# Kernel tuning notes

Measured on AMD Instinct MI355X. Metric: run time of the kernel, lower is better.

## Reference

```python
import jax, jax.numpy as jnp
import numpy as np

B, C, N, H = 8, 256, 1024, 8

def setup_inputs() -> dict:
    key = jax.random.key(0)
    ks = jax.random.split(key, 6)
    x = jax.random.normal(ks[0], (B, C, 3, N), jnp.float32)
    scale = 1.0 / np.sqrt(C).astype(np.float32)
    Wq = jax.random.normal(ks[1], (C, C), jnp.float32) * scale
    Wk = jax.random.normal(ks[2], (C, C), jnp.float32) * scale
    Wv = jax.random.normal(ks[3], (C, C), jnp.float32) * scale
    Wp = jax.random.normal(ks[4], (C, C), jnp.float32) * scale
    mask = jax.random.randint(ks[5], (B, N), 0, 2).astype(bool)  # True = padded
    return {"x": x, "Wq": Wq, "Wk": Wk, "Wv": Wv, "Wp": Wp, "mask": mask}

def _vn_linear(W, x):
    # VNLinear: channel-mixing linear (no bias) over the C axis of [B, C, 3, N]
    return jnp.einsum('oc,bcdn->bodn', W, x)

def _to_heads(t):
    # [B, C, 3, N] -> [B, H, N, (C//H)*3]
    hd = C // H
    return t.reshape(B, H, hd, 3, N).transpose(0, 1, 4, 2, 3).reshape(B, H, N, hd * 3)

def reference(x, Wq, Wk, Wv, Wp, mask):
    hd = C // H
    D = hd * 3
    q = _to_heads(_vn_linear(Wq, x))
    k = _to_heads(_vn_linear(Wk, x))
    v = _to_heads(_vn_linear(Wv, x))
    att = jnp.einsum('bhnd,bhmd->bhnm', q, k) * (1.0 / np.sqrt(D).astype(np.float32))
    att = jnp.where(mask[:, None, None, :], -jnp.inf, att)
    att = jax.nn.softmax(att, axis=-1)
    y = jnp.einsum('bhnm,bhmd->bhnd', att, v)
    # [B, H, N, D] -> [B, H, D, N] -> [B, H, hd, 3, N] -> [B, C, 3, N]
    y = y.transpose(0, 1, 3, 2).reshape(B, H, hd, 3, N).reshape(B, C, 3, N)
    return _vn_linear(Wp, y)
```

## Files before the change

kernel.cpp:

```cpp
#include <hip/hip_runtime.h>
#include <hip/hip_bf16.h>
#include <math.h>

#define B_ 8
#define C_ 256
#define N_ 1024
#define H_ 8
#define DH 96
#define BHN (C_*3*N_)
#define SC 0.10206207261596575f
#define SCL2 0.14722193f

typedef _Float16 half8 __attribute__((ext_vector_type(8)));
typedef float f32x4 __attribute__((ext_vector_type(4)));
typedef float f32x16 __attribute__((ext_vector_type(16)));

typedef __attribute__((address_space(1))) void gvoid;
typedef __attribute__((address_space(3))) void lvoid;
__device__ inline void gl_lds16(const _Float16* g, _Float16* l) {
  __builtin_amdgcn_global_load_lds((gvoid*)g, (lvoid*)l, 16, 0, 0);
}

__device__ inline float ex2(float x) { return __builtin_amdgcn_exp2f(x); }

typedef __fp16 fp16x2 __attribute__((ext_vector_type(2)));
union H2U { fp16x2 h2; unsigned u; };
__device__ inline unsigned pkh(float a, float b) {
  H2U x; x.h2 = __builtin_amdgcn_cvt_pkrtz(a, b); return x.u;
}
union PF { half8 v; unsigned u[4]; };

__device__ inline void plswap(unsigned& a, unsigned& b) {
  asm volatile("v_permlane32_swap_b32 %0, %1" : "+v"(a), "+v"(b));
}

__global__ __launch_bounds__(256) void prep_kernel(
    const float* __restrict__ x, _Float16* __restrict__ XT,
    const float* __restrict__ Wq, const float* __restrict__ Wk,
    const float* __restrict__ Wv, const float* __restrict__ Wp,
    _Float16* __restrict__ Wh, const unsigned* __restrict__ mraw,
    unsigned long long* __restrict__ mb) {
  if (blockIdx.z == 8) {
    int bid = blockIdx.y * 48 + blockIdx.x;
    if (bid < 128) {
      int idx = bid * 256 + threadIdx.x;
      int e0 = idx * 8;
      const float* src = (e0 < 65536) ? Wq
                       : (e0 < 131072) ? Wk
                       : (e0 < 196608) ? Wv : Wp;
      int off = e0 & 65535;
      float4 a = *(const float4*)&src[off];
      float4 b = *(const float4*)&src[off + 4];
      _Float16 t[8] = {(_Float16)a.x, (_Float16)a.y, (_Float16)a.z,
                       (_Float16)a.w, (_Float16)b.x, (_Float16)b.y,
                       (_Float16)b.z, (_Float16)b.w};
      *(uint4*)&Wh[e0] = *(uint4*)t;
    } else if (bid == 128) {
      __shared__ int notI, notF;
      if (threadIdx.x == 0) { notI = 0; notF = 0; }
      __syncthreads();
      int li = 0, lf = 0;
      for (int i = threadIdx.x; i < 2048; i += 256) {
        unsigned w = mraw[i];
        if (w > 1u) li = 1;
        if (w != 0u && w != 0x3F800000u) lf = 1;
      }
      if (li) atomicOr(&notI, 1);
      if (lf) atomicOr(&notF, 1);
      __syncthreads();
      const int tid = threadIdx.x;
      if (tid < 128) {
        int base = tid * 64;
        unsigned long long bits = 0;
        if (!notI) {
          for (int j = 0; j < 64; ++j)
            bits |= (unsigned long long)(mraw[base + j] & 1u) << j;
        } else if (!notF) {
          for (int j = 0; j < 64; ++j)
            bits |= (unsigned long long)(mraw[base + j] != 0u ? 1 : 0) << j;
        } else {
          const unsigned char* m8 = (const unsigned char*)mraw;
          for (int j = 0; j < 64; ++j)
            bits |= (unsigned long long)(m8[base + j] ? 1 : 0) << j;
        }
        mb[tid] = bits;
      }
    }
    return;
  }

  __shared__ _Float16 T[64][65];
  const int m0 = blockIdx.x * 64;
  const int c0 = blockIdx.y * 64;
  const int b = blockIdx.z;
  const float* xb = x + (size_t)b * BHN;
  _Float16* ob = XT + (size_t)b * BHN;
  const int t = threadIdx.x;
#pragma unroll
  for (int i = 0; i < 16; ++i) {
    int e = t + i * 256;
    int c = e >> 6, m = e & 63;
    T[m][c] = (_Float16)xb[(size_t)(c0 + c) * 3072 + m0 + m];
  }
  __syncthreads();
#pragma unroll
  for (int i = 0; i < 2; ++i) {
    int e = t + i * 256;
    int m = e >> 3, ch = e & 7;
    _Float16 tmp[8];
#pragma unroll
    for (int j = 0; j < 8; ++j) tmp[j] = T[m][ch * 8 + j];
    *(uint4*)&ob[(size_t)(m0 + m) * 256 + c0 + ch * 8] = *(uint4*)tmp;
  }
}

template <int MODE>
__global__ __launch_bounds__(256, 4) void mgemm_kernel(
    const _Float16* __restrict__ Wh, int woff,
    const _Float16* __restrict__ Xn,
    _Float16* __restrict__ O0, _Float16* __restrict__ O1,
    _Float16* __restrict__ O2, float* __restrict__ Of, int nw) {
  const int zz = blockIdx.z;
  const int w = zz % nw;
  const int b = zz / nw;
  const _Float16* Wb = Wh + (size_t)(woff + w) * 65536;
  const _Float16* Bb = Xn + (size_t)b * BHN;
  const int o0 = blockIdx.y * 128;
  const int bn0 = blockIdx.x * 128;

  __shared__ __align__(16) _Float16 Ah[8192];
  __shared__ __align__(16) _Float16 Bh[8192];

  const int tid = threadIdx.x;
  const int wave = tid >> 6;
  const int lane = tid & 63;
  const int lg = lane >> 4, ll = lane & 15;
  const int wm = wave >> 1, wn = wave & 1;

  f32x4 acc[4][4];
#pragma unroll
  for (int mi = 0; mi < 4; ++mi)
#pragma unroll
    for (int ni = 0; ni < 4; ++ni) acc[mi][ni] = (f32x4){0.f, 0.f, 0.f, 0.f};

  for (int k0 = 0; k0 < 256; k0 += 64) {
#pragma unroll
    for (int i = 0; i < 4; ++i) {
      int e = tid + i * 256;
      int r = e >> 3, cch = e & 7;
      int srcc = cch ^ (r & 7);
      _Float16* dst = &Ah[(size_t)(i * 256 + wave * 64) * 8];
      gl_lds16(Wb + (size_t)(o0 + r) * 256 + k0 + srcc * 8, dst);
      _Float16* dstb = &Bh[(size_t)(i * 256 + wave * 64) * 8];
      gl_lds16(Bb + (size_t)(bn0 + r) * 256 + k0 + srcc * 8, dstb);
    }
    __syncthreads();
#pragma unroll
    for (int kk = 0; kk < 2; ++kk) {
      half8 af[4], bf[4];
#pragma unroll
      for (int mi = 0; mi < 4; ++mi) {
        int row = wm * 64 + mi * 16 + ll;
        int ch = (kk * 4 + lg) ^ (row & 7);
        af[mi] = *(const half8*)&Ah[row * 64 + ch * 8];
      }
#pragma unroll
      for (int ni = 0; ni < 4; ++ni) {
        int row = wn * 64 + ni * 16 + ll;
        int ch = (kk * 4 + lg) ^ (row & 7);
        bf[ni] = *(const half8*)&Bh[row * 64 + ch * 8];
      }
#pragma unroll
      for (int mi = 0; mi < 4; ++mi)
#pragma unroll
        for (int ni = 0; ni < 4; ++ni)
          acc[mi][ni] = __builtin_amdgcn_mfma_f32_16x16x32_f16(
              af[mi], bf[ni], acc[mi][ni], 0, 0, 0);
    }
    __syncthreads();
  }

#pragma unroll
  for (int mi = 0; mi < 4; ++mi) {
#pragma unroll
    for (int ni = 0; ni < 4; ++ni) {
      int o = o0 + wm * 64 + mi * 16 + lg * 4;
      int mcol = bn0 + wn * 64 + ni * 16 + ll;
      if constexpr (MODE == 1) {
        float* Ofb = Of + (size_t)b * BHN;
#pragma unroll
        for (int r = 0; r < 4; ++r)
          Ofb[(size_t)(o + r) * 3072 + mcol] = acc[mi][ni][r];
      } else {
        const int h = o >> 5, i = o & 31;
        const int dd = mcol >> 10, tok = mcol & 1023;
        const size_t bh8 = (size_t)(b * 8 + h);
        if (w == 2) {
          int tt = tok >> 6, kk = tok & 63;
          int kt = kk >> 4, hi2 = (kk >> 3) & 1, e = kk & 7;
          size_t base = ((((bh8 * 16 + tt) * 4 + kt) * 3 + dd) * 512) +
                        (size_t)i * 16 + hi2 * 8 + e;
#pragma unroll
          for (int r = 0; r < 4; ++r)
            O2[base + r * 16] = (_Float16)acc[mi][ni][r];
        } else {
          int dperm = dd * 32 + i;
          int pp = dperm >> 3, j0 = i & 7;
          int ks = pp >> 1, hif = pp & 1;
          float qs = (w == 0) ? SCL2 : 1.0f;
          _Float16 t4[4];
#pragma unroll
          for (int r = 0; r < 4; ++r) t4[r] = (_Float16)(acc[mi][ni][r] * qs);
          size_t idx;
          if (w == 0) {
            idx = ((bh8 * 32 + (tok >> 5)) * 6 + ks) * 512 +
                  (size_t)(tok & 31) * 16 + hif * 8 + j0;
            *(uint2*)&O0[idx] = *(uint2*)t4;
          } else {
            idx = ((bh8 * 16 + (tok >> 6)) * 6 + ks) * 1024 +
                  (size_t)(tok & 63) * 16 + hif * 8 + j0;
            *(uint2*)&O1[idx] = *(uint2*)t4;
          }
        }
      }
    }
  }
}

__global__ __launch_bounds__(256, 2) void attn_kernel(
    const _Float16* __restrict__ Qp, const _Float16* __restrict__ Kp,
    const _Float16* __restrict__ Vp,
    const unsigned long long* __restrict__ mbits,
    _Float16* __restrict__ yT) {
  const int gid = blockIdx.x;
  const int bh = gid & 63;
  const int qt = gid >> 6;
  const int b = bh >> 3, h = bh & 7;
  const int n0 = qt * 128;

  const int tid = threadIdx.x;
  const int lane = tid & 63;
  const int wave = tid >> 6;
  const int hi = lane >> 5;
  const int lq = lane & 31;
  const int wq0 = wave * 32;

  const size_t bh8 = (size_t)(b * 8 + h);
  const int lo16 = lq * 16 + hi * 8;

  const _Float16* Qb = Qp + (bh8 * 32 + (qt * 4 + wave)) * 6 * 512 + lo16;
  half8 qf[6];
#pragma unroll
  for (int ks = 0; ks < 6; ++ks) qf[ks] = *(const half8*)(Qb + ks * 512);

  const _Float16* Kh = Kp + bh8 * 98304 + lo16;
  const _Float16* Vh = Vp + bh8 * 98304 + lo16;

  half8 kf[6][2];
  auto loadK = [&](int t) {
    const _Float16* Kt = Kh + t * 6144;
#pragma unroll
    for (int ks = 0; ks < 6; ++ks) {
      kf[ks][0] = *(const half8*)(Kt + ks * 1024);
      kf[ks][1] = *(const half8*)(Kt + ks * 1024 + 512);
    }
  };
  loadK(0);

  float M = 0.f, Lh = 0.f;
  f32x16 yacc[3];
#pragma unroll
  for (int dt = 0; dt < 3; ++dt)
#pragma unroll
    for (int r = 0; r < 16; ++r) yacc[dt][r] = 0.f;

  for (int t = 0; t < 16; ++t) {
    const _Float16* Vt = Vh + t * 6144;
    half8 vf[4][3];
#pragma unroll
    for (int kt = 0; kt < 4; ++kt)
#pragma unroll
      for (int dt = 0; dt < 3; ++dt)
        vf[kt][dt] = *(const half8*)(Vt + (kt * 3 + dt) * 512);

    const unsigned long long m64 = mbits[b * 16 + t];

    f32x16 s[2];
#pragma unroll
    for (int r = 0; r < 16; ++r) { s[0][r] = 0.f; s[1][r] = 0.f; }
    __builtin_amdgcn_s_setprio(1);
#pragma unroll
    for (int ks = 0; ks < 6; ++ks) {
      s[0] = __builtin_amdgcn_mfma_f32_32x32x16_f16(kf[ks][0], qf[ks], s[0],
                                                    0, 0, 0);
      s[1] = __builtin_amdgcn_mfma_f32_32x32x16_f16(kf[ks][1], qf[ks], s[1],
                                                    0, 0, 0);
    }
    __builtin_amdgcn_s_setprio(0);

    if (t + 1 < 16) loadK(t + 1);

    float mx = -1e30f;
#pragma unroll
    for (int nt = 0; nt < 2; ++nt) {
      unsigned wm = (unsigned)(m64 >> (nt * 32 + 4 * hi));
#pragma unroll
      for (int r = 0; r < 16; ++r) {
        float sv = s[nt][r];
        sv = ((wm >> ((r & 3) + 8 * (r >> 2))) & 1u) ? -1e30f : sv;
        s[nt][r] = sv;
        mx = fmaxf(mx, sv);
      }
    }
    if (__any(mx > M + 12.f)) {
      float mx2 = fmaxf(mx, __shfl_xor(mx, 32));
      float newM = fmaxf(M, mx2);
      float corr = ex2(M - newM);
      M = newM;
      Lh *= corr;
#pragma unroll
      for (int dt = 0; dt < 3; ++dt)
#pragma unroll
        for (int r = 0; r < 16; ++r) yacc[dt][r] *= corr;
    }
    float psum = 0.f;
#pragma unroll
    for (int nt = 0; nt < 2; ++nt)
#pragma unroll
      for (int r = 0; r < 16; ++r) {
        float p = ex2(s[nt][r] - M);
        s[nt][r] = p;
        psum += p;
      }
    Lh += psum;

#pragma unroll
    for (int nt = 0; nt < 2; ++nt) {
#pragma unroll
      for (int hf = 0; hf < 2; ++hf) {
        const int bs = hf * 8;
        unsigned A0 = pkh(s[nt][bs + 0], s[nt][bs + 1]);
        unsigned A1 = pkh(s[nt][bs + 2], s[nt][bs + 3]);
        unsigned B0 = pkh(s[nt][bs + 4], s[nt][bs + 5]);
        unsigned B1 = pkh(s[nt][bs + 6], s[nt][bs + 7]);
        plswap(A0, B0);
        plswap(A1, B1);
        PF pf;
        pf.u[0] = A0;
        pf.u[1] = A1;
        pf.u[2] = B0;
        pf.u[3] = B1;
        const int kt = nt * 2 + hf;
        __builtin_amdgcn_s_setprio(1);
#pragma unroll
        for (int dt = 0; dt < 3; ++dt)
          yacc[dt] = __builtin_amdgcn_mfma_f32_32x32x16_f16(
              vf[kt][dt], pf.v, yacc[dt], 0, 0, 0);
        __builtin_amdgcn_s_setprio(0);
      }
    }
  }

  float L = Lh + __shfl_xor(Lh, 32);
  float inv = (L > 0.f) ? 1.f / L : 0.f;
  _Float16* yb = yT + (size_t)b * BHN;
#pragma unroll
  for (int dt = 0; dt < 3; ++dt) {
    _Float16* rowp =
        yb + (size_t)(dt * 1024 + n0 + wq0 + lq) * 256 + h * 32 + hi * 4;
#pragma unroll
    for (int g = 0; g < 4; ++g) {
      _Float16 t4[4];
#pragma unroll
      for (int j = 0; j < 4; ++j)
        t4[j] = (_Float16)(yacc[dt][g * 4 + j] * inv);
      *(uint2*)(rowp + g * 8) = *(uint2*)t4;
    }
  }
}

extern "C" void kernel_launch(void* const* d_in, const int* in_sizes, int n_in,
                              void* d_out, int out_size, void* d_ws,
                              size_t ws_size, hipStream_t stream) {
  const float* x = (const float*)d_in[0];
  const float* Wq = (const float*)d_in[1];
  const float* Wk = (const float*)d_in[2];
  const float* Wv = (const float*)d_in[3];
  const float* Wp = (const float*)d_in[4];
  const unsigned* mask = (const unsigned*)d_in[5];
  float* out = (float*)d_out;

  _Float16* Wh = (_Float16*)d_ws;
  _Float16* XT = Wh + 4 * 65536;
  _Float16* Qp = XT + (size_t)B_ * BHN;
  _Float16* Kp = Qp + (size_t)B_ * BHN;
  _Float16* Vp = Kp + (size_t)B_ * BHN;
  _Float16* yT = Vp + (size_t)B_ * BHN;
  unsigned long long* mb = (unsigned long long*)(yT + (size_t)B_ * BHN);

  prep_kernel<<<dim3(48, 4, 9), 256, 0, stream>>>(x, XT, Wq, Wk, Wv, Wp, Wh,
                                                  mask, mb);

  dim3 g1(24, 2, B_ * 3);
  mgemm_kernel<0><<<g1, 256, 0, stream>>>(Wh, 0, XT, Qp, Kp, Vp, nullptr, 3);

  attn_kernel<<<dim3(512), 256, 0, stream>>>(Qp, Kp, Vp, mb, yT);

  dim3 g3(24, 2, B_);
  mgemm_kernel<1><<<g3, 256, 0, stream>>>(Wh, 3, yT, nullptr, nullptr, nullptr,
                                          out, 1);
}
```

Measured before the change: 90.29 us.

## Compact unpadded keys/values to front and skip fully masked key tiles

The prep kernel computes a per-batch prefix-sum permutation that places unpadded tokens first and padded tokens last. It also writes the number of non-empty 64-key tiles and per-tile mask bits for that order. The projection GEMM scatters K and V rows into this compacted order, and the attention loop runs only over the live tiles instead of all 16. With about half the keys masked, this roughly halves attention work. It adds a serial scan in one block and indirect index loads in the GEMM epilogue.

Measured after the change: 94.59 us. 1.05x slower.

```diff
diff --git a/kernel.cpp b/kernel.cpp
--- a/kernel.cpp
+++ b/kernel.cpp
@@ -39,11 +39,13 @@
     const float* __restrict__ Wq, const float* __restrict__ Wk,
     const float* __restrict__ Wv, const float* __restrict__ Wp,
     _Float16* __restrict__ Wh, const unsigned* __restrict__ mraw,
-    unsigned long long* __restrict__ mb) {
+    unsigned long long* __restrict__ mb, int* __restrict__ pos,
+    int* __restrict__ ntArr) {
   if (blockIdx.z == 8) {
     int bid = blockIdx.y * 48 + blockIdx.x;
+    const int tid = threadIdx.x;
     if (bid < 128) {
-      int idx = bid * 256 + threadIdx.x;
+      int idx = bid * 256 + tid;
       int e0 = idx * 8;
       const float* src = (e0 < 65536) ? Wq
                        : (e0 < 131072) ? Wk
@@ -57,10 +59,11 @@
       *(uint4*)&Wh[e0] = *(uint4*)t;
     } else if (bid == 128) {
       __shared__ int notI, notF;
-      if (threadIdx.x == 0) { notI = 0; notF = 0; }
+      __shared__ int cnts[256];
+      if (tid == 0) { notI = 0; notF = 0; }
       __syncthreads();
       int li = 0, lf = 0;
-      for (int i = threadIdx.x; i < 2048; i += 256) {
+      for (int i = tid; i < 2048; i += 256) {
         unsigned w = mraw[i];
         if (w > 1u) li = 1;
         if (w != 0u && w != 0x3F800000u) lf = 1;
@@ -68,22 +71,45 @@
       if (li) atomicOr(&notI, 1);
       if (lf) atomicOr(&notF, 1);
       __syncthreads();
-      const int tid = threadIdx.x;
-      if (tid < 128) {
-        int base = tid * 64;
-        unsigned long long bits = 0;
-        if (!notI) {
-          for (int j = 0; j < 64; ++j)
-            bits |= (unsigned long long)(mraw[base + j] & 1u) << j;
-        } else if (!notF) {
-          for (int j = 0; j < 64; ++j)
-            bits |= (unsigned long long)(mraw[base + j] != 0u ? 1 : 0) << j;
-        } else {
-          const unsigned char* m8 = (const unsigned char*)mraw;
-          for (int j = 0; j < 64; ++j)
-            bits |= (unsigned long long)(m8[base + j] ? 1 : 0) << j;
+      const int nI = notI, nF = notF;
+      auto ispad = [&](int idx) -> int {
+        if (!nI) return (int)(mraw[idx] & 1u);
+        if (!nF) return (mraw[idx] != 0u) ? 1 : 0;
+        return ((const unsigned char*)mraw)[idx] ? 1 : 0;
+      };
+      const int gb = tid >> 5, gi = tid & 31;
+      const int tbase = gb * 1024 + gi * 32;
+      int cloc = 0;
+      for (int j = 0; j < 32; ++j) cloc += 1 - ispad(tbase + j);
+      cnts[tid] = cloc;
+      __syncthreads();
+      int pre = 0, tot = 0;
+      for (int k2 = 0; k2 < 32; ++k2) {
+        int v = cnts[gb * 32 + k2];
+        if (k2 < gi) pre += v;
+        tot += v;
+      }
+      int pu = pre;
+      int pm = tot + (gi * 32 - pre);
+      for (int j = 0; j < 32; ++j) {
+        int tok = gi * 32 + j;
+        int pd = ispad(tbase + j);
+        int p = pd ? pm++ : pu++;
+        pos[gb * 1024 + tok] = p;
+      }
+      if (gi == 0) {
+        int nt = (tot + 63) >> 6;
+        if (nt == 0) nt = 1;
+        ntArr[gb] = nt;
+        int rem = tot & 63;
+        for (int t = 0; t < 16; ++t) {
+          unsigned long long bits;
+          if (t < nt - 1) bits = 0ULL;
+          else if (t == nt - 1)
+            bits = (rem == 0 && tot > 0) ? 0ULL : (~0ULL << rem);
+          else bits = ~0ULL;
+          mb[gb * 16 + t] = bits;
         }
-        mb[tid] = bits;
       }
     }
     return;
@@ -117,7 +143,7 @@
 template <int MODE>
 __global__ __launch_bounds__(256, 4) void mgemm_kernel(
     const _Float16* __restrict__ Wh, int woff,
-    const _Float16* __restrict__ Xn,
+    const _Float16* __restrict__ Xn, const int* __restrict__ pos,
     _Float16* __restrict__ O0, _Float16* __restrict__ O1,
     _Float16* __restrict__ O2, float* __restrict__ Of, int nw) {
   const int zz = blockIdx.z;
@@ -196,31 +222,36 @@
         const int dd = mcol >> 10, tok = mcol & 1023;
         const size_t bh8 = (size_t)(b * 8 + h);
         if (w == 2) {
-          int tt = tok >> 6, kk = tok & 63;
+          int ctok = pos[b * 1024 + tok];
+          int tt = ctok >> 6, kk = ctok & 63;
           int kt = kk >> 4, hi2 = (kk >> 3) & 1, e = kk & 7;
           size_t base = ((((bh8 * 16 + tt) * 4 + kt) * 3 + dd) * 512) +
                         (size_t)i * 16 + hi2 * 8 + e;
 #pragma unroll
           for (int r = 0; r < 4; ++r)
             O2[base + r * 16] = (_Float16)acc[mi][ni][r];
+        } else if (w == 1) {
+          int ctok = pos[b * 1024 + tok];
+          int dperm = dd * 32 + i;
+          int pp = dperm >> 3, j0 = i & 7;
+          int ks = pp >> 1, hif = pp & 1;
+          _Float16 t4[4];
+#pragma unroll
+          for (int r = 0; r < 4; ++r) t4[r] = (_Float16)acc[mi][ni][r];
+          size_t idx = ((bh8 * 16 + (ctok >> 6)) * 6 + ks) * 1024 +
+                       (size_t)(ctok & 63) * 16 + hif * 8 + j0;
+          *(uint2*)&O1[idx] = *(uint2*)t4;
         } else {
           int dperm = dd * 32 + i;
           int pp = dperm >> 3, j0 = i & 7;
           int ks = pp >> 1, hif = pp & 1;
-          float qs = (w == 0) ? SCL2 : 1.0f;
           _Float16 t4[4];
 #pragma unroll
-          for (int r = 0; r < 4; ++r) t4[r] = (_Float16)(acc[mi][ni][r] * qs);
-          size_t idx;
-          if (w == 0) {
-            idx = ((bh8 * 32 + (tok >> 5)) * 6 + ks) * 512 +
-                  (size_t)(tok & 31) * 16 + hif * 8 + j0;
-            *(uint2*)&O0[idx] = *(uint2*)t4;
-          } else {
-            idx = ((bh8 * 16 + (tok >> 6)) * 6 + ks) * 1024 +
-                  (size_t)(tok & 63) * 16 + hif * 8 + j0;
-            *(uint2*)&O1[idx] = *(uint2*)t4;
-          }
+          for (int r = 0; r < 4; ++r)
+            t4[r] = (_Float16)(acc[mi][ni][r] * SCL2);
+          size_t idx = ((bh8 * 32 + (tok >> 5)) * 6 + ks) * 512 +
+                       (size_t)(tok & 31) * 16 + hif * 8 + j0;
+          *(uint2*)&O0[idx] = *(uint2*)t4;
         }
       }
     }
@@ -231,12 +262,13 @@
     const _Float16* __restrict__ Qp, const _Float16* __restrict__ Kp,
     const _Float16* __restrict__ Vp,
     const unsigned long long* __restrict__ mbits,
-    _Float16* __restrict__ yT) {
+    const int* __restrict__ ntArr, _Float16* __restrict__ yT) {
   const int gid = blockIdx.x;
   const int bh = gid & 63;
   const int qt = gid >> 6;
   const int b = bh >> 3, h = bh & 7;
   const int n0 = qt * 128;
+  const int nt = ntArr[b];
 
   const int tid = threadIdx.x;
   const int lane = tid & 63;
@@ -274,7 +306,7 @@
 #pragma unroll
     for (int r = 0; r < 16; ++r) yacc[dt][r] = 0.f;
 
-  for (int t = 0; t < 16; ++t) {
+  for (int t = 0; t < nt; ++t) {
     const _Float16* Vt = Vh + t * 6144;
     half8 vf[4][3];
 #pragma unroll
@@ -298,17 +330,17 @@
     }
     __builtin_amdgcn_s_setprio(0);
 
-    if (t + 1 < 16) loadK(t + 1);
+    if (t + 1 < nt) loadK(t + 1);
 
     float mx = -1e30f;
 #pragma unroll
-    for (int nt = 0; nt < 2; ++nt) {
-      unsigned wm = (unsigned)(m64 >> (nt * 32 + 4 * hi));
+    for (int nt2 = 0; nt2 < 2; ++nt2) {
+      unsigned wm = (unsigned)(m64 >> (nt2 * 32 + 4 * hi));
 #pragma unroll
       for (int r = 0; r < 16; ++r) {
-        float sv = s[nt][r];
+        float sv = s[nt2][r];
         sv = ((wm >> ((r & 3) + 8 * (r >> 2))) & 1u) ? -1e30f : sv;
-        s[nt][r] = sv;
+        s[nt2][r] = sv;
         mx = fmaxf(mx, sv);
       }
     }
@@ -325,24 +357,24 @@
     }
     float psum = 0.f;
 #pragma unroll
-    for (int nt = 0; nt < 2; ++nt)
+    for (int nt2 = 0; nt2 < 2; ++nt2)
 #pragma unroll
       for (int r = 0; r < 16; ++r) {
-        float p = ex2(s[nt][r] - M);
-        s[nt][r] = p;
+        float p = ex2(s[nt2][r] - M);
+        s[nt2][r] = p;
         psum += p;
       }
     Lh += psum;
 
 #pragma unroll
-    for (int nt = 0; nt < 2; ++nt) {
+    for (int nt2 = 0; nt2 < 2; ++nt2) {
 #pragma unroll
       for (int hf = 0; hf < 2; ++hf) {
         const int bs = hf * 8;
-        unsigned A0 = pkh(s[nt][bs + 0], s[nt][bs + 1]);
-        unsigned A1 = pkh(s[nt][bs + 2], s[nt][bs + 3]);
-        unsigned B0 = pkh(s[nt][bs + 4], s[nt][bs + 5]);
-        unsigned B1 = pkh(s[nt][bs + 6], s[nt][bs + 7]);
+        unsigned A0 = pkh(s[nt2][bs + 0], s[nt2][bs + 1]);
+        unsigned A1 = pkh(s[nt2][bs + 2], s[nt2][bs + 3]);
+        unsigned B0 = pkh(s[nt2][bs + 4], s[nt2][bs + 5]);
+        unsigned B1 = pkh(s[nt2][bs + 6], s[nt2][bs + 7]);
         plswap(A0, B0);
         plswap(A1, B1);
         PF pf;
@@ -350,7 +382,7 @@
         pf.u[1] = A1;
         pf.u[2] = B0;
         pf.u[3] = B1;
-        const int kt = nt * 2 + hf;
+        const int kt = nt2 * 2 + hf;
         __builtin_amdgcn_s_setprio(1);
 #pragma unroll
         for (int dt = 0; dt < 3; ++dt)
@@ -397,16 +429,19 @@
   _Float16* Vp = Kp + (size_t)B_ * BHN;
   _Float16* yT = Vp + (size_t)B_ * BHN;
   unsigned long long* mb = (unsigned long long*)(yT + (size_t)B_ * BHN);
+  int* posArr = (int*)(mb + 128);
+  int* ntArr = posArr + 8192;
 
   prep_kernel<<<dim3(48, 4, 9), 256, 0, stream>>>(x, XT, Wq, Wk, Wv, Wp, Wh,
-                                                  mask, mb);
+                                                  mask, mb, posArr, ntArr);
 
   dim3 g1(24, 2, B_ * 3);
-  mgemm_kernel<0><<<g1, 256, 0, stream>>>(Wh, 0, XT, Qp, Kp, Vp, nullptr, 3);
-
-  attn_kernel<<<dim3(512), 256, 0, stream>>>(Qp, Kp, Vp, mb, yT);
+  mgemm_kernel<0><<<g1, 256, 0, stream>>>(Wh, 0, XT, posArr, Qp, Kp, Vp,
+                                          nullptr, 3);
+
+  attn_kernel<<<dim3(512), 256, 0, stream>>>(Qp, Kp, Vp, mb, ntArr, yT);
 
   dim3 g3(24, 2, B_);
-  mgemm_kernel<1><<<g3, 256, 0, stream>>>(Wh, 3, yT, nullptr, nullptr, nullptr,
-                                          out, 1);
-}
+  mgemm_kernel<1><<<g3, 256, 0, stream>>>(Wh, 3, yT, posArr, nullptr, nullptr,
+                                          nullptr, out, 1);
+}
```
